# Optimization experiments

Hardware: AMD Instinct MI355X
Metric: run time of the kernel (lower is better)

Reference implementation:

```python
import math
import jax, jax.numpy as jnp
import numpy as np

IMG = 512; P = 16; CIN = 3; COUT = 3; E = 768; NHEADS = 12; L = 8
NPH = IMG // P            # 32 patches per side
N = NPH * NPH             # 1024 tokens (must match learned 1024x1024 attn bias)
HD = E // NHEADS          # 64
INTER = min(E // 2, 128)  # 128, OutputProjection intermediate
EPS = 1e-5


def _sin_pe(n_h, n_w, d):
    # faithful port of get_2d_sinusoidal_encoding (second half stays zero)
    pe = np.zeros((n_h, n_w, d), dtype=np.float32)
    dq, dh = d // 4, d // 2
    div = np.exp(np.arange(0, dq, 2, dtype=np.float32) * (-math.log(10000.0) / dq))
    pr = np.arange(n_h, dtype=np.float32)[:, None]
    pc = np.arange(n_w, dtype=np.float32)[:, None]
    pe[:, :, 0:dq:2] = np.sin(pr * div)[:, None, :]
    pe[:, :, 1:dq:2] = np.cos(pr * div)[:, None, :]
    pe[:, :, dq:dh:2] = np.sin(pc * div)[None, :, :]
    pe[:, :, dq + 1:dh:2] = np.cos(pc * div)[None, :, :]
    return jnp.asarray(pe.reshape(-1, d))


def _ln(x, g, b):
    m = x.mean(-1, keepdims=True)
    v = ((x - m) ** 2).mean(-1, keepdims=True)
    return (x - m) * jax.lax.rsqrt(v + EPS) * g + b


def setup_inputs():
    key = jax.random.key(0)
    ks = iter(jax.random.split(key, 32))
    def nrm(shape, scale=0.02):
        return jax.random.normal(next(ks), shape, jnp.float32) * scale
    return {
        'x': jax.random.normal(next(ks), (2, CIN, IMG, IMG), jnp.float32),
        'conv_w': nrm((E, CIN, P, P)), 'conv_b': jnp.zeros((E,), jnp.float32),
        'ln1_g': jnp.ones((L, E), jnp.float32), 'ln1_b': jnp.zeros((L, E), jnp.float32),
        'qkv_w': nrm((L, 3 * E, E)),
        'proj_w': nrm((L, E, E)), 'proj_b': jnp.zeros((L, E), jnp.float32),
        'attn_bias': jax.random.normal(next(ks), (L, N, N), jnp.float32),  # torch.randn init
        'ln2_g': jnp.ones((L, E), jnp.float32), 'ln2_b': jnp.zeros((L, E), jnp.float32),
        'mlp_w1': nrm((L, 2 * E, E)), 'mlp_b1': jnp.zeros((L, 2 * E), jnp.float32),
        'mlp_w2': nrm((L, E, 2 * E)), 'mlp_b2': jnp.zeros((L, E), jnp.float32),
        'op_w1': nrm((INTER, E)), 'op_b1': jnp.zeros((INTER,), jnp.float32),
        'op_w2': nrm((P * P * COUT, INTER)), 'op_b2': jnp.zeros((P * P * COUT,), jnp.float32),
        'ag_wg': nrm((1, COUT), 0.2), 'ag_bng_w': jnp.ones((), jnp.float32), 'ag_bng_b': jnp.zeros((), jnp.float32),
        'ag_wx': nrm((1, CIN), 0.2), 'ag_bnx_w': jnp.ones((), jnp.float32), 'ag_bnx_b': jnp.zeros((), jnp.float32),
        'ag_psi_w': jnp.full((), 0.5, jnp.float32), 'ag_psi_b': jnp.zeros((), jnp.float32),
    }


def reference(x, conv_w, conv_b, ln1_g, ln1_b, qkv_w, proj_w, proj_b, attn_bias,
              ln2_g, ln2_b, mlp_w1, mlp_b1, mlp_w2, mlp_b2,
              op_w1, op_b1, op_w2, op_b2,
              ag_wg, ag_bng_w, ag_bng_b, ag_wx, ag_bnx_w, ag_bnx_b, ag_psi_w, ag_psi_b):
    B = x.shape[0]
    # --- VisionTransformerInput: patch-embed conv (stride == kernel) as reshape+GEMM ---
    xp = x.reshape(B, CIN, NPH, P, NPH, P).transpose(0, 2, 4, 1, 3, 5).reshape(B, N, CIN * P * P)
    t = xp @ conv_w.reshape(E, -1).T + conv_b
    t = t + _sin_pe(NPH, NPH, E)[None]

    # --- encoder blocks (scan over stacked per-layer params) ---
    def block(t, p):
        y = _ln(t, p['ln1_g'], p['ln1_b'])
        qkv = (y @ p['qkv_w'].T).reshape(B, N, 3, NHEADS, HD).transpose(2, 0, 3, 1, 4)
        q, k, v = qkv[0], qkv[1], qkv[2]
        s = jnp.einsum('bhnd,bhmd->bhnm', q, k) / math.sqrt(HD)
        # NOTE: relative_position_bias is computed but never added in the source (dead code);
        # only the learned (N,N) bias parameter is added.
        s = s + p['attn_bias'][None, None]
        a = jax.nn.softmax(s, axis=-1)
        o = jnp.einsum('bhnm,bhmd->bhnd', a, v).transpose(0, 2, 1, 3).reshape(B, N, E)
        o = o @ p['proj_w'].T + p['proj_b']
        t = t + (y + o)  # MHA has an extra internal residual (out = x + out) in the source
        h = _ln(t, p['ln2_g'], p['ln2_b'])
        h = jax.nn.gelu(h @ p['mlp_w1'].T + p['mlp_b1'], approximate=False) @ p['mlp_w2'].T + p['mlp_b2']
        return t + h, None

    stacked = {'ln1_g': ln1_g, 'ln1_b': ln1_b, 'qkv_w': qkv_w, 'proj_w': proj_w,
               'proj_b': proj_b, 'attn_bias': attn_bias, 'ln2_g': ln2_g, 'ln2_b': ln2_b,
               'mlp_w1': mlp_w1, 'mlp_b1': mlp_b1, 'mlp_w2': mlp_w2, 'mlp_b2': mlp_b2}
    t, _ = jax.lax.scan(block, t, stacked)

    # --- OutputProjection: MLP -> Fold -> attention gate -> (identity) interpolate ---
    h = jax.nn.relu(t @ op_w1.T + op_b1) @ op_w2.T + op_b2  # (B, N, C*P*P)
    # nn.Fold(kernel=stride=P): columns interpreted as (C, P, P)
    g = h.reshape(B, NPH, NPH, COUT, P, P).transpose(0, 3, 1, 4, 2, 5).reshape(B, COUT, IMG, IMG)
    inv = 1.0 / math.sqrt(1.0 + EPS)  # BatchNorm eval: running_mean=0, running_var=1
    g1 = jnp.einsum('bchw,oc->bohw', g, ag_wg) * (inv * ag_bng_w) + ag_bng_b
    x1 = jnp.einsum('bchw,oc->bohw', x, ag_wx) * (inv * ag_bnx_w) + ag_bnx_b
    psi = jax.nn.sigmoid(jax.nn.relu(g1 + x1) * ag_psi_w + ag_psi_b)
    out = g * (x * psi)  # x * att_gate's psi == skip_gated; then x_fold * skip_gated
    # F.interpolate to (output_size, output_size) with output_size == image_size: identity
    return out
```

## Files before the change

kernel.cpp:

```cpp
#include <hip/hip_runtime.h>
#include <math.h>

typedef unsigned short u16;
typedef unsigned int u32;
typedef __attribute__((ext_vector_type(8))) short bf16x8;
typedef __attribute__((ext_vector_type(16))) float f32x16;
typedef __attribute__((ext_vector_type(4))) float f4v;
typedef __attribute__((ext_vector_type(4))) u32 u32x4;

#define MFMA(a, b, c) __builtin_amdgcn_mfma_f32_32x32x16_bf16(a, b, c, 0, 0, 0)

#define SYNC_STEP() do {                                   \
    asm volatile("s_waitcnt vmcnt(0)" ::: "memory");       \
    __builtin_amdgcn_s_barrier();                          \
    __builtin_amdgcn_sched_barrier(0);                     \
} while (0)

#define SYNC_CNT_LIT(nlit) do {                                    \
    asm volatile("s_waitcnt vmcnt(" #nlit ")" ::: "memory");       \
    __builtin_amdgcn_s_barrier();                                  \
    __builtin_amdgcn_sched_barrier(0);                             \
} while (0)

__device__ __forceinline__ float bf2f(u16 h) { return __uint_as_float(((u32)h) << 16); }

__device__ __forceinline__ void split2(float v, u16& h, u16& l) {
    u32 u = __float_as_uint(v);
    u32 hr = (u + 0x7FFFu + ((u >> 16) & 1u)) & 0xFFFF0000u;
    h = (u16)(hr >> 16);
    float lf = v - __uint_as_float(hr);
    u32 ul = __float_as_uint(lf);
    l = (u16)((ul + 0x7FFFu + ((ul >> 16) & 1u)) >> 16);
}

__device__ __forceinline__ u32 cvtpk(float lo, float hi) {
    u32 r;
    asm("v_cvt_pk_bf16_f32 %0, %1, %2" : "=v"(r) : "v"(lo), "v"(hi));
    return r;
}

__device__ __forceinline__ void swap32(u32& a, u32& b, int hi) {
    u32 ta = (u32)__shfl_xor((int)a, 32);
    u32 tb = (u32)__shfl_xor((int)b, 32);
    u32 na = hi ? tb : a;
    u32 nb = hi ? b : ta;
    a = na; b = nb;
}

__device__ __forceinline__ void repack(const f32x16& v, int base, int hi, bf16x8& fh, bf16x8& fl) {
    float p0 = v[base + 0], p1 = v[base + 1], p2 = v[base + 2], p3 = v[base + 3];
    float p4 = v[base + 4], p5 = v[base + 5], p6 = v[base + 6], p7 = v[base + 7];
    u32 X0 = cvtpk(p0, p1), X1 = cvtpk(p2, p3), X4 = cvtpk(p4, p5), X5 = cvtpk(p6, p7);
    float r0 = p0 - __uint_as_float(X0 << 16);
    float r1 = p1 - __uint_as_float(X0 & 0xFFFF0000u);
    float r2 = p2 - __uint_as_float(X1 << 16);
    float r3 = p3 - __uint_as_float(X1 & 0xFFFF0000u);
    float r4 = p4 - __uint_as_float(X4 << 16);
    float r5 = p5 - __uint_as_float(X4 & 0xFFFF0000u);
    float r6 = p6 - __uint_as_float(X5 << 16);
    float r7 = p7 - __uint_as_float(X5 & 0xFFFF0000u);
    u32 L0 = cvtpk(r0, r1), L1 = cvtpk(r2, r3), L4 = cvtpk(r4, r5), L5 = cvtpk(r6, r7);
    swap32(X0, X4, hi); swap32(X1, X5, hi);
    swap32(L0, L4, hi); swap32(L1, L5, hi);
    u32x4 th = {X0, X1, X4, X5};
    u32x4 tl = {L0, L1, L4, L5};
    fh = __builtin_bit_cast(bf16x8, th);
    fl = __builtin_bit_cast(bf16x8, tl);
}

__global__ __launch_bounds__(256) void pe_kernel(float* __restrict__ pe) {
    int idx = blockIdx.x * 256 + threadIdx.x;
    int n = idx / 768, d = idx - n * 768;
    float v = 0.0f;
    if (d < 384) {
        int pos = (d < 192) ? (n >> 5) : (n & 31);
        int dd  = (d < 192) ? d : d - 192;
        int j2  = dd & ~1;
        float dv  = expf((float)j2 * (-9.210340371976184f / 192.0f));
        float ang = (float)pos * dv;
        v = (dd & 1) ? cosf(ang) : sinf(ang);
    }
    pe[idx] = v;
}

__global__ __launch_bounds__(256) void gather_kernel(const float* __restrict__ x,
                                                     u16* __restrict__ xph,
                                                     u16* __restrict__ xpl) {
    int idx = blockIdx.x * 256 + threadIdx.x;
    int m = idx / 768, col = idx - m * 768;
    int b = m >> 10, n = m & 1023;
    int ci = col >> 8, rem = col & 255;
    int pr = rem >> 4, pc = rem & 15;
    int hh = ((n >> 5) << 4) + pr;
    int ww = ((n & 31) << 4) + pc;
    float v = x[(((size_t)(b * 3 + ci) * 512) + hh) * 512 + ww];
    split2(v, xph[idx], xpl[idx]);
}

__global__ __launch_bounds__(256) void fsplit(const float* __restrict__ in,
                                              u16* __restrict__ h, u16* __restrict__ l, int n4) {
    int i = blockIdx.x * 256 + threadIdx.x;
    if (i >= n4) return;
    float4 v = ((const float4*)in)[i];
    int o = i * 4;
    split2(v.x, h[o], l[o]);
    split2(v.y, h[o + 1], l[o + 1]);
    split2(v.z, h[o + 2], l[o + 2]);
    split2(v.w, h[o + 3], l[o + 3]);
}

__global__ __launch_bounds__(256) void wsplit_layer(const float* __restrict__ qkvw,
                                                    const float* __restrict__ projw,
                                                    const float* __restrict__ w1,
                                                    const float* __restrict__ w2,
                                                    u16* __restrict__ wh, u16* __restrict__ wl) {
    int i4 = blockIdx.x * 256 + threadIdx.x;
    if (i4 >= 1179648) return;
    size_t idx = (size_t)i4 * 4;
    const float* src; size_t off;
    if (idx < 1769472)      { src = qkvw;  off = idx; }
    else if (idx < 2359296) { src = projw; off = idx - 1769472; }
    else if (idx < 3538944) { src = w1;    off = idx - 2359296; }
    else                    { src = w2;    off = idx - 3538944; }
    float4 v = *(const float4*)(src + off);
    split2(v.x, wh[idx], wl[idx]);
    split2(v.y, wh[idx + 1], wl[idx + 1]);
    split2(v.z, wh[idx + 2], wl[idx + 2]);
    split2(v.w, wh[idx + 3], wl[idx + 3]);
}

__global__ __launch_bounds__(256) void btrans(const float* __restrict__ src, float* __restrict__ dst) {
    __shared__ float tl[32][33];
    int bx = blockIdx.x & 31, by = blockIdx.x >> 5;
    int tx = threadIdx.x & 31, ty = threadIdx.x >> 5;
#pragma unroll
    for (int j = 0; j < 4; ++j)
        tl[ty + j * 8][tx] = src[(size_t)(by * 32 + ty + j * 8) * 1024 + bx * 32 + tx];
    __syncthreads();
#pragma unroll
    for (int j = 0; j < 4; ++j)
        dst[(size_t)(bx * 32 + ty + j * 8) * 1024 + by * 32 + tx] = tl[tx][ty + j * 8];
}

__global__ __launch_bounds__(256) void ln_kernel(const float* __restrict__ x,
                                                 const float* __restrict__ g,
                                                 const float* __restrict__ b,
                                                 u16* __restrict__ yh, u16* __restrict__ yl) {
    int row = blockIdx.x, tid = threadIdx.x;
    int wid = tid >> 6, lane = tid & 63;
    const float* xr = x + (size_t)row * 768;
    float v0 = xr[tid], v1 = xr[tid + 256], v2 = xr[tid + 512];
    __shared__ float ws[8];
    float sum = v0 + v1 + v2;
#pragma unroll
    for (int off = 32; off > 0; off >>= 1) sum += __shfl_xor(sum, off);
    if (lane == 0) ws[wid] = sum;
    __syncthreads();
    float mean = (ws[0] + ws[1] + ws[2] + ws[3]) * (1.0f / 768.0f);
    float d0 = v0 - mean, d1 = v1 - mean, d2 = v2 - mean;
    float vs = d0 * d0 + d1 * d1 + d2 * d2;
#pragma unroll
    for (int off = 32; off > 0; off >>= 1) vs += __shfl_xor(vs, off);
    if (lane == 0) ws[4 + wid] = vs;
    __syncthreads();
    float rstd = rsqrtf((ws[4] + ws[5] + ws[6] + ws[7]) * (1.0f / 768.0f) + 1e-5f);
    size_t o = (size_t)row * 768;
    split2(d0 * rstd * g[tid]       + b[tid],       yh[o + tid],       yl[o + tid]);
    split2(d1 * rstd * g[tid + 256] + b[tid + 256], yh[o + tid + 256], yl[o + tid + 256]);
    split2(d2 * rstd * g[tid + 512] + b[tid + 512], yh[o + tid + 512], yl[o + tid + 512]);
}

__device__ __forceinline__ int mrow(int r) { return (r + (r >> 2)) & 3; }

template <int MODE>
__global__ __launch_bounds__(256, 2) void gemm_sp(const u16* __restrict__ Ah, const u16* __restrict__ Al,
                                                  const u16* __restrict__ Bh, const u16* __restrict__ Bl,
                                                  const float* __restrict__ bias,
                                                  const float* __restrict__ res,
                                                  const float* __restrict__ auxf,
                                                  const u16* __restrict__ auxh, const u16* __restrict__ auxl,
                                                  float* __restrict__ C, u16* __restrict__ Ch, u16* __restrict__ Cl,
                                                  int M, int N, int K, int nby) {
    __shared__ u16 SH[36864];
    u16* As = SH;
    u16* Bs = SH + 12288;
    int tid = threadIdx.x;
    int wid = tid >> 6, lane = tid & 63;
    int hi = lane >> 5;
    int lq = lane & 31;

    int nwg = gridDim.x;
    int q8 = nwg >> 3;
    int swz = (blockIdx.x & 7) * q8 + (blockIdx.x >> 3);
    int cb = swz / nby, rb = swz - cb * nby;
    int m0 = rb * 64, n0 = cb * 128;

    f32x16 acc0 = {}, acc1 = {};

    auto stage = [&](int buf, int kt) {
#pragma unroll
        for (int c = 0; c < 2; ++c) {
            const u16* G = c ? Al : Ah;
            int row = wid * 16 + (lane >> 2);
            int ch = (lane & 3) ^ mrow(row);
            const u16* g = G + (size_t)(m0 + row) * K + kt + ch * 8;
            __builtin_amdgcn_global_load_lds((const __attribute__((address_space(1))) u32*)g,
                                             (__attribute__((address_space(3))) u32*)&As[(buf * 2 + c) * 2048 + (wid * 16) * 32],
                                             16, 0, 0);
        }
#pragma unroll
        for (int c = 0; c < 2; ++c) {
            const u16* G = c ? Bl : Bh;
#pragma unroll
            for (int j = 0; j < 2; ++j) {
                int row = wid * 32 + j * 16 + (lane >> 2);
                int ch = (lane & 3) ^ mrow(row);
                const u16* g = G + (size_t)(n0 + row) * K + kt + ch * 8;
                __builtin_amdgcn_global_load_lds((const __attribute__((address_space(1))) u32*)g,
                                                 (__attribute__((address_space(3))) u32*)&Bs[(buf * 2 + c) * 4096 + (wid * 32 + j * 16) * 32],
                                                 16, 0, 0);
            }
        }
    };

    int ar  = (wid >> 1) * 32 + lq;
    int br0 = (wid & 1) * 64 + lq;
    int br1 = br0 + 32;

    auto compute = [&](int buf) {
#pragma unroll
        for (int kc = 0; kc < 2; ++kc) {
            int gc = (kc << 1) | hi;
            int oA  = ar  * 32 + ((gc ^ mrow(ar))  << 3);
            int oB0 = br0 * 32 + ((gc ^ mrow(br0)) << 3);
            int oB1 = br1 * 32 + ((gc ^ mrow(br1)) << 3);
            bf16x8 ah  = *(const bf16x8*)(As + (buf * 2 + 0) * 2048 + oA);
            bf16x8 al  = *(const bf16x8*)(As + (buf * 2 + 1) * 2048 + oA);
            bf16x8 b0h = *(const bf16x8*)(Bs + (buf * 2 + 0) * 4096 + oB0);
            bf16x8 b0l = *(const bf16x8*)(Bs + (buf * 2 + 1) * 4096 + oB0);
            bf16x8 b1h = *(const bf16x8*)(Bs + (buf * 2 + 0) * 4096 + oB1);
            bf16x8 b1l = *(const bf16x8*)(Bs + (buf * 2 + 1) * 4096 + oB1);
            acc0 = MFMA(ah, b0h, acc0);
            acc0 = MFMA(ah, b0l, acc0);
            acc0 = MFMA(al, b0h, acc0);
            acc1 = MFMA(ah, b1h, acc1);
            acc1 = MFMA(ah, b1l, acc1);
            acc1 = MFMA(al, b1h, acc1);
        }
    };

    int nk = K >> 5;
    stage(0, 0);
    stage(1, 32);
    int t = 0;
    for (; t < nk - 1; ++t) {
        SYNC_CNT_LIT(6);
        if (t + 2 < nk) stage((t + 2) % 3, (t + 2) << 5);
        compute(t % 3);
    }
    SYNC_STEP();
    compute(t % 3);

    auto epi = [&](const f32x16& a, int ncol) {
        int col = n0 + ncol + lq;
        int rb2 = m0 + (wid >> 1) * 32 + (hi << 2);
#pragma unroll
        for (int r = 0; r < 16; ++r) {
            int row = rb2 + (r & 3) + ((r >> 2) << 3);
            float v = a[r];
            size_t o = (size_t)row * N + col;
            if (MODE == 1) C[o] = v + bias[col] + auxf[(size_t)(row & 1023) * N + col];
            else if (MODE == 2) C[o] = res[o] + (bf2f(auxh[o]) + bf2f(auxl[o])) + v + bias[col];
            else if (MODE == 4) C[o] = res[o] + v + bias[col];
            else if (MODE == 5) {
                v += bias[col];
                v = fmaxf(v, 0.0f);
                split2(v, Ch[o], Cl[o]);
            }
            else if (MODE == 6) C[o] = v + bias[col];
        }
    };
    epi(acc0, (wid & 1) * 64);
    epi(acc1, (wid & 1) * 64 + 32);
}

template <int MODE>
__global__ __launch_bounds__(256, 2) void gemm_sq(const u16* __restrict__ Ah, const u16* __restrict__ Al,
                                                  const u16* __restrict__ Bh, const u16* __restrict__ Bl,
                                                  const float* __restrict__ bias,
                                                  u16* __restrict__ Ch, u16* __restrict__ Cl,
                                                  u16* __restrict__ Cth, u16* __restrict__ Ctl,
                                                  int M, int N, int K, int nby) {
    __shared__ u16 SH[32768];
    int tid = threadIdx.x;
    int wid = tid >> 6, lane = tid & 63;
    int hi = lane >> 5;
    int lq = lane & 31;
    int wm = wid >> 1, wn = wid & 1;

    int nwg = gridDim.x;
    int q8 = nwg >> 3;
    int swz = (blockIdx.x & 7) * q8 + (blockIdx.x >> 3);
    int cb = swz / nby, rb = swz - cb * nby;
    int m0 = rb * 128, n0 = cb * 128;

    f32x16 acc00 = {}, acc01 = {}, acc10 = {}, acc11 = {};

    const u16* srcs[4] = {Ah, Al, Bh, Bl};
    auto stage = [&](int buf, int kt) {
        const u16* G = srcs[wid];
        int rbase = (wid < 2) ? m0 : n0;
#pragma unroll
        for (int i = 0; i < 8; ++i) {
            int row = i * 16 + (lane >> 2);
            int ch = (lane & 3) ^ mrow(row);
            const u16* g = G + (size_t)(rbase + row) * K + kt + ch * 8;
            __builtin_amdgcn_global_load_lds((const __attribute__((address_space(1))) u32*)g,
                                             (__attribute__((address_space(3))) u32*)&SH[buf * 16384 + wid * 4096 + i * 512],
                                             16, 0, 0);
        }
    };

    int ar0 = wm * 64 + lq, ar1 = ar0 + 32;
    int br0 = wn * 64 + lq, br1 = br0 + 32;

    auto compute = [&](int buf) {
        const u16* SAh = SH + buf * 16384;
        const u16* SAl = SAh + 4096;
        const u16* SBh = SAl + 4096;
        const u16* SBl = SBh + 4096;
#pragma unroll
        for (int kc = 0; kc < 2; ++kc) {
            int gc = (kc << 1) | hi;
            int oA0 = ar0 * 32 + ((gc ^ mrow(ar0)) << 3);
            int oA1 = ar1 * 32 + ((gc ^ mrow(ar1)) << 3);
            int oB0 = br0 * 32 + ((gc ^ mrow(br0)) << 3);
            int oB1 = br1 * 32 + ((gc ^ mrow(br1)) << 3);
            bf16x8 a0h = *(const bf16x8*)(SAh + oA0);
            bf16x8 a0l = *(const bf16x8*)(SAl + oA0);
            bf16x8 a1h = *(const bf16x8*)(SAh + oA1);
            bf16x8 a1l = *(const bf16x8*)(SAl + oA1);
            bf16x8 b0h = *(const bf16x8*)(SBh + oB0);
            bf16x8 b0l = *(const bf16x8*)(SBl + oB0);
            bf16x8 b1h = *(const bf16x8*)(SBh + oB1);
            bf16x8 b1l = *(const bf16x8*)(SBl + oB1);
            acc00 = MFMA(a0h, b0h, acc00);
            acc00 = MFMA(a0h, b0l, acc00);
            acc00 = MFMA(a0l, b0h, acc00);
            acc01 = MFMA(a0h, b1h, acc01);
            acc01 = MFMA(a0h, b1l, acc01);
            acc01 = MFMA(a0l, b1h, acc01);
            acc10 = MFMA(a1h, b0h, acc10);
            acc10 = MFMA(a1h, b0l, acc10);
            acc10 = MFMA(a1l, b0h, acc10);
            acc11 = MFMA(a1h, b1h, acc11);
            acc11 = MFMA(a1h, b1l, acc11);
            acc11 = MFMA(a1l, b1h, acc11);
        }
    };

    int nk = K >> 5;
    stage(0, 0);
    for (int t = 0; t < nk; ++t) {
        SYNC_STEP();
        if (t + 1 < nk) stage((t + 1) & 1, (t + 1) << 5);
        compute(t & 1);
    }

    if (MODE == 7 && n0 >= 1536) {
        int bb = m0 >> 10;
        int nbase = m0 & 1023;
#pragma unroll
        for (int P = 0; P < 2; ++P) {
            __syncthreads();
            if (wm == P) {
                auto scat = [&](const f32x16& a, int fm, int fn) {
                    int c = wn * 64 + fn * 32 + lq;
                    int rbl = fm * 32 + (hi << 2);
#pragma unroll
                    for (int r = 0; r < 16; ++r) {
                        int rr = rbl + (r & 3) + ((r >> 2) << 3);
                        u16 hv, lv;
                        split2(a[r], hv, lv);
                        SH[c * 68 + rr] = hv;
                        SH[8704 + c * 68 + rr] = lv;
                    }
                };
                scat(acc00, 0, 0); scat(acc01, 0, 1); scat(acc10, 1, 0); scat(acc11, 1, 1);
            }
            __syncthreads();
#pragma unroll
            for (int pass = 0; pass < 4; ++pass) {
                int c2 = pass * 32 + (tid >> 3);
                int ch8 = tid & 7;
                int hcol = (n0 - 1536) + c2;
                int h2 = hcol >> 6, hd = hcol & 63;
                size_t dst = ((size_t)(bb * 12 + h2) * 64 + hd) * 1024 + nbase + P * 64 + ch8 * 8;
                int so = c2 * 68 + ch8 * 8;
                u32x4 ph = {*(const u32*)&SH[so], *(const u32*)&SH[so + 2],
                            *(const u32*)&SH[so + 4], *(const u32*)&SH[so + 6]};
                u32x4 pl = {*(const u32*)&SH[8704 + so], *(const u32*)&SH[8704 + so + 2],
                            *(const u32*)&SH[8704 + so + 4], *(const u32*)&SH[8704 + so + 6]};
                *(u32x4*)(Cth + dst) = ph;
                *(u32x4*)(Ctl + dst) = pl;
            }
        }
        return;
    }

    auto epi = [&](const f32x16& a, int fm, int fn) {
        int col = n0 + wn * 64 + fn * 32 + lq;
        int rb2 = m0 + wm * 64 + fm * 32 + (hi << 2);
#pragma unroll
        for (int r = 0; r < 16; ++r) {
            int row = rb2 + (r & 3) + ((r >> 2) << 3);
            float v = a[r];
            if (MODE == 3) {
                size_t o = (size_t)row * N + col;
                v += bias[col];
                v = 0.5f * v * (1.0f + erff(v * 0.70710678118654752f));
                split2(v, Ch[o], Cl[o]);
            } else if (MODE == 7) {
                size_t o7 = (size_t)row * 1536 + col;
                split2(v, Ch[o7], Cl[o7]);
            }
        }
    };
    epi(acc00, 0, 0); epi(acc01, 0, 1); epi(acc10, 1, 0); epi(acc11, 1, 1);
}

__global__ __launch_bounds__(256, 2) void attn_mfma(const u16* __restrict__ qh, const u16* __restrict__ ql,
                                                    const u16* __restrict__ vth, const u16* __restrict__ vtl,
                                                    const float* __restrict__ biasT,
                                                    u16* __restrict__ oh, u16* __restrict__ ol) {
    __shared__ u16 smem[2][2][4][2048];
    int tid = threadIdx.x;
    int wid = tid >> 6, lane = tid & 63;
    int s = wid & 1, p = wid >> 1;
    int lq = lane & 31;
    int hi = lane >> 5;
    int id = blockIdx.x;
    int xcd = id & 7;
    int j = id >> 3;
    int bh = xcd * 3 + (j >> 4);
    int qt = j & 15;
    int b = bh / 12, h = bh % 12;
    int bq0 = qt * 64;
    int gq = bq0 + s * 32 + lq;

    bf16x8 qfh[4], qfl[4];
    {
        size_t qo = (size_t)(b * 1024 + gq) * 1536 + h * 64 + hi * 8;
#pragma unroll
        for (int ks = 0; ks < 4; ++ks) {
            qfh[ks] = *(const bf16x8*)(qh + qo + ks * 16);
            qfl[ks] = *(const bf16x8*)(ql + qo + ks * 16);
        }
    }

    f32x16 oa = {}, ob = {};
    float m_i = -1e30f, l_i = 0.0f;

    auto stage = [&](int buf, int kb) {
        if (s == 0) {
#pragma unroll
            for (int c = 0; c < 2; ++c) {
                const u16* G = c ? ql : qh;
#pragma unroll
                for (int i = 0; i < 4; ++i) {
                    int r = 8 * i + (lane >> 3);
                    int cl = (lane & 7) ^ (r & 7);
                    const u16* g = G + (size_t)(b * 1024 + kb + r) * 1536 + 768 + h * 64 + cl * 8;
                    __builtin_amdgcn_global_load_lds((const __attribute__((address_space(1))) u32*)g,
                                                     (__attribute__((address_space(3))) u32*)&smem[p][buf][c][i * 512],
                                                     16, 0, 0);
                }
            }
        } else {
#pragma unroll
            for (int c = 0; c < 2; ++c) {
                const u16* G = c ? vtl : vth;
#pragma unroll
                for (int i = 0; i < 4; ++i) {
                    int r = 16 * i + (lane >> 2);
                    int cl = (lane & 3) ^ ((r >> 1) & 3);
                    const u16* g = G + ((size_t)(b * 12 + h) * 64 + r) * 1024 + kb + cl * 8;
                    __builtin_amdgcn_global_load_lds((const __attribute__((address_space(1))) u32*)g,
                                                     (__attribute__((address_space(3))) u32*)&smem[p][buf][2 + c][i * 512],
                                                     16, 0, 0);
                }
            }
        }
    };

    auto loadBias = [&](float (&bb)[16], int kb) {
        const float* bbase = biasT + (size_t)(kb + 4 * hi) * 1024 + gq;
#pragma unroll
        for (int g2 = 0; g2 < 4; ++g2)
#pragma unroll
            for (int q = 0; q < 4; ++q)
                bb[g2 * 4 + q] = bbase[(size_t)(g2 * 8 + q) * 1024];
    };

    auto compute = [&](int buf, const float (&bb)[16]) {
        const u16* Kh = &smem[p][buf][0][0];
        const u16* Kl = &smem[p][buf][1][0];
        const u16* Vh = &smem[p][buf][2][0];
        const u16* Vl = &smem[p][buf][3][0];
        f32x16 s0 = {}, s1 = {};
        __builtin_amdgcn_s_setprio(1);
#pragma unroll
        for (int ks = 0; ks < 2; ++ks) {
            int offA = lq * 64 + (((2 * ks + hi) ^ (lq & 7)) << 3);
            int offB = lq * 64 + (((2 * (ks + 2) + hi) ^ (lq & 7)) << 3);
            bf16x8 khA = *(const bf16x8*)(Kh + offA);
            bf16x8 klA = *(const bf16x8*)(Kl + offA);
            bf16x8 khB = *(const bf16x8*)(Kh + offB);
            bf16x8 klB = *(const bf16x8*)(Kl + offB);
            s0 = MFMA(khA, qfh[ks], s0);
            s1 = MFMA(khB, qfh[ks + 2], s1);
            s0 = MFMA(khA, qfl[ks], s0);
            s1 = MFMA(khB, qfl[ks + 2], s1);
            s0 = MFMA(klA, qfh[ks], s0);
            s1 = MFMA(klB, qfh[ks + 2], s1);
        }
        __builtin_amdgcn_s_setprio(0);
        bf16x8 vf[2][4];
#pragma unroll
        for (int kslot = 0; kslot < 2; ++kslot) {
            int offa = lq * 32 + (((2 * kslot + hi) ^ ((lq >> 1) & 3)) << 3);
            vf[kslot][0] = *(const bf16x8*)(Vh + offa);
            vf[kslot][1] = *(const bf16x8*)(Vh + offa + 1024);
            vf[kslot][2] = *(const bf16x8*)(Vl + offa);
            vf[kslot][3] = *(const bf16x8*)(Vl + offa + 1024);
        }
        f32x16 sa;
#pragma unroll
        for (int r = 0; r < 16; ++r) sa[r] = (s0[r] + s1[r]) * 0.125f + bb[r];
        float m01 = fmaxf(sa[0], sa[1]),  m23 = fmaxf(sa[2], sa[3]);
        float m45 = fmaxf(sa[4], sa[5]),  m67 = fmaxf(sa[6], sa[7]);
        float m89 = fmaxf(sa[8], sa[9]),  mab = fmaxf(sa[10], sa[11]);
        float mcd = fmaxf(sa[12], sa[13]), mef = fmaxf(sa[14], sa[15]);
        float pm = fmaxf(fmaxf(fmaxf(m01, m23), fmaxf(m45, m67)),
                         fmaxf(fmaxf(m89, mab), fmaxf(mcd, mef)));
        pm = fmaxf(pm, __shfl_xor(pm, 32));
        if (__any(pm > m_i + 8.0f)) {
            float mnew = fmaxf(m_i, pm);
            float scl = __expf(m_i - mnew);
            m_i = mnew;
            l_i *= scl;
#pragma unroll
            for (int r = 0; r < 16; ++r) {
                int qr = (r & 3) + 8 * (r >> 2) + 4 * hi;
                float fr = __shfl(scl, qr);
                oa[r] *= fr; ob[r] *= fr;
            }
        }
        float ls = 0.0f;
#pragma unroll
        for (int r = 0; r < 16; ++r) { sa[r] = __expf(sa[r] - m_i); ls += sa[r]; }
        ls += __shfl_xor(ls, 32);
        l_i += ls;
        __builtin_amdgcn_s_setprio(1);
#pragma unroll
        for (int kslot = 0; kslot < 2; ++kslot) {
            bf16x8 ph, pl;
            repack(sa, kslot * 8, hi, ph, pl);
            oa = MFMA(ph, vf[kslot][0], oa);
            oa = MFMA(ph, vf[kslot][2], oa);
            oa = MFMA(pl, vf[kslot][0], oa);
            ob = MFMA(ph, vf[kslot][1], ob);
            ob = MFMA(ph, vf[kslot][3], ob);
            ob = MFMA(pl, vf[kslot][1], ob);
        }
        __builtin_amdgcn_s_setprio(0);
    };

    float bbA[16], bbB[16];
    stage(0, p * 32);
    loadBias(bbA, p * 32);
    for (int ss = 0; ss < 16; ss += 2) {
        SYNC_STEP();
        if (ss + 1 < 16) { stage(1, (2 * (ss + 1) + p) * 32); loadBias(bbB, (2 * (ss + 1) + p) * 32); }
        compute(0, bbA);
        SYNC_STEP();
        if (ss + 2 < 16) { stage(0, (2 * (ss + 2) + p) * 32); loadBias(bbA, (2 * (ss + 2) + p) * 32); }
        compute(1, bbB);
    }
    __syncthreads();

    float* mlb = (float*)((char*)smem + 32768);
    mlb[((s * 2 + p) * 2 + 0) * 32 + lq] = m_i;
    mlb[((s * 2 + p) * 2 + 1) * 32 + lq] = l_i;
    __syncthreads();
    float mo  = mlb[((s * 2 + (p ^ 1)) * 2 + 0) * 32 + lq];
    float lo_ = mlb[((s * 2 + (p ^ 1)) * 2 + 1) * 32 + lq];
    float M = fmaxf(m_i, mo);
    float ea = __expf(m_i - M), eb = __expf(mo - M);
    float L = ea * l_i + eb * lo_;
    float f = ea / L;
    float frv[16];
#pragma unroll
    for (int r = 0; r < 16; ++r) frv[r] = __shfl(f, (r & 3) + 8 * (r >> 2) + 4 * hi);
    float* ox = (float*)((char*)smem + s * 8192);
    if (p == 1) {
#pragma unroll
        for (int r = 0; r < 16; ++r) {
            int qr = (r & 3) + 8 * (r >> 2) + 4 * hi;
            ox[qr * 64 + lq] = oa[r] * frv[r];
            ox[qr * 64 + 32 + lq] = ob[r] * frv[r];
        }
    }
    __syncthreads();
    if (p == 0) {
#pragma unroll
        for (int r = 0; r < 16; ++r) {
            int qr = (r & 3) + 8 * (r >> 2) + 4 * hi;
            float va = oa[r] * frv[r] + ox[qr * 64 + lq];
            float vb = ob[r] * frv[r] + ox[qr * 64 + 32 + lq];
            size_t d = (size_t)(b * 1024 + bq0 + s * 32 + qr) * 768 + h * 64;
            split2(va, oh[d + lq], ol[d + lq]);
            split2(vb, oh[d + 32 + lq], ol[d + 32 + lq]);
        }
    }
}

__global__ __launch_bounds__(256) void fold_gate(const float* __restrict__ hbuf,
                                                 const float* __restrict__ xin,
                                                 const float* __restrict__ wg,
                                                 const float* __restrict__ bngw,
                                                 const float* __restrict__ bngb,
                                                 const float* __restrict__ wx,
                                                 const float* __restrict__ bnxw,
                                                 const float* __restrict__ bnxb,
                                                 const float* __restrict__ psiw,
                                                 const float* __restrict__ psib,
                                                 float* __restrict__ out) {
    int idx = blockIdx.x * 256 + threadIdx.x;
    int b = idx >> 18;
    int rem = idx & 262143;
    int hh = rem >> 9, ww = rem & 511;
    int n = ((hh >> 4) << 5) + (ww >> 4);
    int pr = hh & 15, pc = ww & 15;
    const float* hrow = hbuf + (size_t)(b * 1024 + n) * 768 + pr * 16 + pc;
    float g0 = hrow[0], g1 = hrow[256], g2 = hrow[512];
    size_t xoff = ((size_t)(b * 3) * 512 + hh) * 512 + ww;
    float x0 = xin[xoff], x1 = xin[xoff + 262144], x2 = xin[xoff + 524288];
    float inv = rsqrtf(1.0f + 1e-5f);
    float gg = (g0 * wg[0] + g1 * wg[1] + g2 * wg[2]) * inv * bngw[0] + bngb[0];
    float xx = (x0 * wx[0] + x1 * wx[1] + x2 * wx[2]) * inv * bnxw[0] + bnxb[0];
    float z = gg + xx;
    z = z > 0.0f ? z : 0.0f;
    float psi = 1.0f / (1.0f + expf(-(z * psiw[0] + psib[0])));
    out[xoff]          = g0 * x0 * psi;
    out[xoff + 262144] = g1 * x1 * psi;
    out[xoff + 524288] = g2 * x2 * psi;
}

extern "C" void kernel_launch(void* const* d_in, const int* in_sizes, int n_in,
                              void* d_out, int out_size, void* d_ws, size_t ws_size,
                              hipStream_t stream) {
    (void)in_sizes; (void)n_in; (void)out_size; (void)ws_size;
    const float* x       = (const float*)d_in[0];
    const float* conv_w  = (const float*)d_in[1];
    const float* conv_b  = (const float*)d_in[2];
    const float* ln1_g   = (const float*)d_in[3];
    const float* ln1_b   = (const float*)d_in[4];
    const float* qkv_w   = (const float*)d_in[5];
    const float* proj_w  = (const float*)d_in[6];
    const float* proj_b  = (const float*)d_in[7];
    const float* attn_bs = (const float*)d_in[8];
    const float* ln2_g   = (const float*)d_in[9];
    const float* ln2_b   = (const float*)d_in[10];
    const float* mlp_w1  = (const float*)d_in[11];
    const float* mlp_b1  = (const float*)d_in[12];
    const float* mlp_w2  = (const float*)d_in[13];
    const float* mlp_b2  = (const float*)d_in[14];
    const float* op_w1   = (const float*)d_in[15];
    const float* op_b1   = (const float*)d_in[16];
    const float* op_w2   = (const float*)d_in[17];
    const float* op_b2   = (const float*)d_in[18];
    const float* ag_wg   = (const float*)d_in[19];
    const float* ag_bngw = (const float*)d_in[20];
    const float* ag_bngb = (const float*)d_in[21];
    const float* ag_wx   = (const float*)d_in[22];
    const float* ag_bnxw = (const float*)d_in[23];
    const float* ag_bnxb = (const float*)d_in[24];
    const float* ag_psiw = (const float*)d_in[25];
    const float* ag_psib = (const float*)d_in[26];
    float* out = (float*)d_out;

    char* w8 = (char*)d_ws;
    float* t     = (float*)(w8);
    u16* yh      = (u16*)(w8 + 6291456);
    u16* yl      = (u16*)(w8 + 9437184);
    u16* ath     = (u16*)(w8 + 12582912);
    u16* atl     = (u16*)(w8 + 15728640);
    u16* mh      = (u16*)(w8 + 18874368);
    u16* ml      = (u16*)(w8 + 25165824);
    u16* qh      = (u16*)(w8 + 31457280);
    u16* ql      = (u16*)(w8 + 37748736);
    u16* wh      = (u16*)(w8 + 44040192);
    u16* wl      = (u16*)(w8 + 53477376);
    float* biasT = (float*)(w8 + 62914560);
    float* pe  = (float*)qh;
    u16* xph = mh; u16* xpl = ml;
    u16* vth = mh; u16* vtl = ml;
    float* oph2 = (float*)qh;
    u16* o1h = ath; u16* o1l = atl;

    const size_t W_QKV = 0, W_PROJ = 1769472, W_MLP1 = 2359296, W_MLP2 = 3538944;

    pe_kernel<<<3072, 256, 0, stream>>>(pe);
    gather_kernel<<<6144, 256, 0, stream>>>(x, xph, xpl);
    fsplit<<<576, 256, 0, stream>>>(conv_w, wh, wl, 147456);
    gemm_sp<1><<<192, 256, 0, stream>>>(xph, xpl, wh, wl, conv_b, nullptr, pe,
                                        nullptr, nullptr, t, nullptr, nullptr, 2048, 768, 768, 32);

    for (int l = 0; l < 8; ++l) {
        wsplit_layer<<<4608, 256, 0, stream>>>(qkv_w + (size_t)l * 1769472, proj_w + (size_t)l * 589824,
                                               mlp_w1 + (size_t)l * 1179648, mlp_w2 + (size_t)l * 1179648,
                                               wh, wl);
        btrans<<<1024, 256, 0, stream>>>(attn_bs + (size_t)l * 1048576, biasT);
        ln_kernel<<<2048, 256, 0, stream>>>(t, ln1_g + l * 768, ln1_b + l * 768, yh, yl);
        gemm_sq<7><<<288, 256, 0, stream>>>(yh, yl, wh + W_QKV, wl + W_QKV, nullptr,
                                            qh, ql, vth, vtl, 2048, 2304, 768, 16);
        attn_mfma<<<384, 256, 0, stream>>>(qh, ql, vth, vtl, biasT, ath, atl);
        gemm_sp<2><<<192, 256, 0, stream>>>(ath, atl, wh + W_PROJ, wl + W_PROJ, proj_b + l * 768,
                                            t, nullptr, yh, yl, t, nullptr, nullptr, 2048, 768, 768, 32);
        ln_kernel<<<2048, 256, 0, stream>>>(t, ln2_g + l * 768, ln2_b + l * 768, yh, yl);
        gemm_sq<3><<<192, 256, 0, stream>>>(yh, yl, wh + W_MLP1, wl + W_MLP1, mlp_b1 + l * 1536,
                                            mh, ml, nullptr, nullptr, 2048, 1536, 768, 16);
        gemm_sp<4><<<192, 256, 0, stream>>>(mh, ml, wh + W_MLP2, wl + W_MLP2, mlp_b2 + l * 768,
                                            t, nullptr, nullptr, nullptr, t, nullptr, nullptr,
                                            2048, 768, 1536, 32);
    }

    fsplit<<<1536, 256, 0, stream>>>(t, yh, yl, 393216);
    fsplit<<<96, 256, 0, stream>>>(op_w1, wh, wl, 24576);
    fsplit<<<96, 256, 0, stream>>>(op_w2, wh + 131072, wl + 131072, 24576);
    gemm_sp<5><<<32, 256, 0, stream>>>(yh, yl, wh, wl, op_b1, nullptr, nullptr,
                                       nullptr, nullptr, nullptr, o1h, o1l, 2048, 128, 768, 32);
    gemm_sp<6><<<192, 256, 0, stream>>>(o1h, o1l, wh + 131072, wl + 131072, op_b2, nullptr,
                                        nullptr, nullptr, nullptr, oph2, nullptr, nullptr,
                                        2048, 768, 128, 32);
    fold_gate<<<2048, 256, 0, stream>>>(oph2, x, ag_wg, ag_bngw, ag_bngb,
                                        ag_wx, ag_bnxw, ag_bnxb, ag_psiw, ag_psib, out);
}
```

Measured before the change: 1.403 ms.

## Single-buffer attention LDS staging to fit four blocks per CU

The attention kernel drops its double-buffered K/V shared-memory stage, halving LDS use, and raises launch bounds from 2 to 4 blocks per CU. K/V staging for the next tile is now issued only after the current tile's compute finishes and an extra barrier, so copy and compute no longer overlap inside a block. The intent is to hide that latency through higher occupancy instead. The tighter register budget under 4-block launch bounds may cause spills.

```diff
diff --git a/kernel.cpp b/kernel.cpp
--- a/kernel.cpp
+++ b/kernel.cpp
@@ -429,11 +429,11 @@
     epi(acc00, 0, 0); epi(acc01, 0, 1); epi(acc10, 1, 0); epi(acc11, 1, 1);
 }
 
-__global__ __launch_bounds__(256, 2) void attn_mfma(const u16* __restrict__ qh, const u16* __restrict__ ql,
+__global__ __launch_bounds__(256, 4) void attn_mfma(const u16* __restrict__ qh, const u16* __restrict__ ql,
                                                     const u16* __restrict__ vth, const u16* __restrict__ vtl,
                                                     const float* __restrict__ biasT,
                                                     u16* __restrict__ oh, u16* __restrict__ ol) {
-    __shared__ u16 smem[2][2][4][2048];
+    __shared__ u16 smem[2][4][2048];
     int tid = threadIdx.x;
     int wid = tid >> 6, lane = tid & 63;
     int s = wid & 1, p = wid >> 1;
@@ -461,7 +461,7 @@
     f32x16 oa = {}, ob = {};
     float m_i = -1e30f, l_i = 0.0f;
 
-    auto stage = [&](int buf, int kb) {
+    auto stage = [&](int kb) {
         if (s == 0) {
 #pragma unroll
             for (int c = 0; c < 2; ++c) {
@@ -472,7 +472,7 @@
                     int cl = (lane & 7) ^ (r & 7);
                     const u16* g = G + (size_t)(b * 1024 + kb + r) * 1536 + 768 + h * 64 + cl * 8;
                     __builtin_amdgcn_global_load_lds((const __attribute__((address_space(1))) u32*)g,
-                                                     (__attribute__((address_space(3))) u32*)&smem[p][buf][c][i * 512],
+                                                     (__attribute__((address_space(3))) u32*)&smem[p][c][i * 512],
                                                      16, 0, 0);
                 }
             }
@@ -486,7 +486,7 @@
                     int cl = (lane & 3) ^ ((r >> 1) & 3);
                     const u16* g = G + ((size_t)(b * 12 + h) * 64 + r) * 1024 + kb + cl * 8;
                     __builtin_amdgcn_global_load_lds((const __attribute__((address_space(1))) u32*)g,
-                                                     (__attribute__((address_space(3))) u32*)&smem[p][buf][2 + c][i * 512],
+                                                     (__attribute__((address_space(3))) u32*)&smem[p][2 + c][i * 512],
                                                      16, 0, 0);
                 }
             }
@@ -502,11 +502,11 @@
                 bb[g2 * 4 + q] = bbase[(size_t)(g2 * 8 + q) * 1024];
     };
 
-    auto compute = [&](int buf, const float (&bb)[16]) {
-        const u16* Kh = &smem[p][buf][0][0];
-        const u16* Kl = &smem[p][buf][1][0];
-        const u16* Vh = &smem[p][buf][2][0];
-        const u16* Vl = &smem[p][buf][3][0];
+    auto compute = [&](const float (&bb)[16]) {
+        const u16* Kh = &smem[p][0][0];
+        const u16* Kl = &smem[p][1][0];
+        const u16* Vh = &smem[p][2][0];
+        const u16* Vl = &smem[p][3][0];
         f32x16 s0 = {}, s1 = {};
         __builtin_amdgcn_s_setprio(1);
 #pragma unroll
@@ -577,19 +577,22 @@
     };
 
     float bbA[16], bbB[16];
-    stage(0, p * 32);
+    stage(p * 32);
     loadBias(bbA, p * 32);
     for (int ss = 0; ss < 16; ss += 2) {
         SYNC_STEP();
-        if (ss + 1 < 16) { stage(1, (2 * (ss + 1) + p) * 32); loadBias(bbB, (2 * (ss + 1) + p) * 32); }
-        compute(0, bbA);
+        if (ss + 1 < 16) loadBias(bbB, (2 * (ss + 1) + p) * 32);
+        compute(bbA);
+        __syncthreads();
+        if (ss + 1 < 16) stage((2 * (ss + 1) + p) * 32);
         SYNC_STEP();
-        if (ss + 2 < 16) { stage(0, (2 * (ss + 2) + p) * 32); loadBias(bbA, (2 * (ss + 2) + p) * 32); }
-        compute(1, bbB);
-    }
-    __syncthreads();
-
-    float* mlb = (float*)((char*)smem + 32768);
+        if (ss + 2 < 16) loadBias(bbA, (2 * (ss + 2) + p) * 32);
+        if (ss + 1 < 16) compute(bbB);
+        __syncthreads();
+        if (ss + 2 < 16) stage((2 * (ss + 2) + p) * 32);
+    }
+
+    float* mlb = (float*)((char*)smem + 16384);
     mlb[((s * 2 + p) * 2 + 0) * 32 + lq] = m_i;
     mlb[((s * 2 + p) * 2 + 1) * 32 + lq] = l_i;
     __syncthreads();
```

Measured after the change: 3.848 ms. 174% more time.
